# Performance work log

Hardware: AMD Instinct MI355X
Metric: run time of the kernel (lower is better)

Reference implementation:

```python
import jax, jax.numpy as jnp
import numpy as np

B, DIN, DOUT, GRID_SIZE, SPLINE_ORDER, N_LAYERS = 4096, 1024, 1024, 8, 3, 2
COEFFS = GRID_SIZE + SPLINE_ORDER  # 11


def _kaiming_uniform(key, shape, fan_in):
    # torch nn.init.kaiming_uniform_ default: a=0 -> gain=sqrt(2), bound=sqrt(3)*gain/sqrt(fan_in)
    bound = float(np.sqrt(6.0 / fan_in))
    return jax.random.uniform(key, shape, jnp.float32, -bound, bound)


def setup_inputs() -> dict:
    key = jax.random.key(0)
    ks = jax.random.split(key, 1 + 3 * N_LAYERS)
    x = jax.random.normal(ks[0], (B, DIN), dtype=jnp.float32)
    # knot grid: arange(-so, gs+so+1)*h + lo, h=(hi-lo)/gs  -> shape [GRID_SIZE+2*SPLINE_ORDER+1]
    h = 2.0 / GRID_SIZE
    grid = jnp.arange(-SPLINE_ORDER, GRID_SIZE + SPLINE_ORDER + 1, dtype=jnp.float32) * h - 1.0
    base_w, spline_w, scaler = [], [], []
    for i in range(N_LAYERS):
        base_w.append(_kaiming_uniform(ks[1 + 3 * i], (DOUT, DIN), DIN))
        spline_w.append(_kaiming_uniform(ks[2 + 3 * i], (DOUT, DIN, COEFFS), DIN * COEFFS))
        scaler.append(_kaiming_uniform(ks[3 + 3 * i], (DOUT, DIN), DIN))
    return {
        "x": x,
        "base_w": jnp.stack(base_w),      # [L, DOUT, DIN]
        "spline_w": jnp.stack(spline_w),  # [L, DOUT, DIN, COEFFS]
        "scaler": jnp.stack(scaler),      # [L, DOUT, DIN]
        "grid": grid,                      # [G]
        "spline_order": SPLINE_ORDER,
    }


def b_splines(x, grid, spline_order):
    # x: (B, DIN) -> bases: (B, DIN, COEFFS) via Cox-de Boor recursion
    x = x[..., None]  # (B, DIN, 1)
    bases = ((x >= grid[:-1]) & (x < grid[1:])).astype(x.dtype)  # order-0 indicators
    for k in range(1, spline_order + 1):
        left = (x - grid[: -(k + 1)]) / (grid[k:-1] - grid[: -(k + 1)])
        right = (grid[k + 1:] - x) / (grid[k + 1:] - grid[1:-k])
        bases = left * bases[..., :-1] + right * bases[..., 1:]
    return bases


def reference(x, base_w, spline_w, scaler, grid, spline_order):
    so = int(spline_order)
    n_layers = base_w.shape[0]
    for i in range(n_layers):
        x = jax.nn.silu(x)                                  # base_activation applied before both branches
        base_out = x @ base_w[i].T                          # (B, DOUT)
        bs = b_splines(x, grid, so)                         # (B, DIN, COEFFS)
        w = spline_w[i] * scaler[i][..., None]              # (DOUT, DIN, COEFFS)
        spline_out = jnp.einsum("bic,oic->bo", bs, w)      # == F.linear on flattened (DIN*COEFFS)
        x = base_out + spline_out
    return x
```

## Files before the change

kernel.cpp:

```cpp
#include <hip/hip_runtime.h>
#include <stdint.h>

#define BATCH 4096
#define DIN 1024
#define DOUT 1024
#define NC 11
#define KD 12288
#define NKNOTS 15

typedef __bf16 bf16x8 __attribute__((ext_vector_type(8)));
typedef float f32x4 __attribute__((ext_vector_type(4)));

__device__ __forceinline__ unsigned short f2bf(float f) {
    unsigned int u = __float_as_uint(f);
    unsigned int r = (u + 0x7FFFu + ((u >> 16) & 1u)) >> 16;
    return (unsigned short)r;
}

__global__ __launch_bounds__(256) void build_A(
    const float* __restrict__ x, const float* __restrict__ P, int np,
    const float* __restrict__ grid, unsigned short* __restrict__ A) {
    __shared__ __align__(16) unsigned short lbs[256 * NC];
    const int tid = threadIdx.x;
    const int b  = blockIdx.x >> 2;
    const int i0 = (blockIdx.x & 3) * 256;
    const int i  = i0 + tid;

    float g[NKNOTS];
#pragma unroll
    for (int j = 0; j < NKNOTS; ++j) g[j] = grid[j];

    float xv = x[(size_t)b * DIN + i];
    for (int p = 0; p < np; ++p)
        xv += P[(size_t)p * BATCH * DIN + (size_t)b * DIN + i];
    const float s = xv / (1.f + __expf(-xv));

    float bs[14];
#pragma unroll
    for (int c = 0; c < 14; ++c) bs[c] = (s >= g[c] && s < g[c + 1]) ? 1.f : 0.f;
#pragma unroll
    for (int k = 1; k <= 3; ++k) {
        const float inv = (k == 1) ? 4.f : (k == 2) ? 2.f : (4.f / 3.f);
#pragma unroll
        for (int c = 0; c < 14 - k; ++c) {
            float left  = (s - g[c]) * inv;
            float right = (g[c + k + 1] - s) * inv;
            bs[c] = left * bs[c] + right * bs[c + 1];
        }
    }

    A[(size_t)b * KD + i] = f2bf(s);
#pragma unroll
    for (int c = 0; c < NC; ++c) lbs[tid * NC + c] = f2bf(bs[c]);
    __syncthreads();

    const uint4* src = (const uint4*)lbs;
    uint4* dst = (uint4*)(A + (size_t)b * KD + DIN + (size_t)i0 * NC);
    for (int j = tid; j < 352; j += 256) dst[j] = src[j];
}

__global__ __launch_bounds__(256) void build_W(
    const float* __restrict__ base_w, const float* __restrict__ spline_w,
    const float* __restrict__ scaler, unsigned short* __restrict__ W) {
    __shared__ __align__(16) unsigned short lw[256 * NC];
    const int tid = threadIdx.x;
    const int o  = blockIdx.x >> 2;
    const int i0 = (blockIdx.x & 3) * 256;
    const int i  = i0 + tid;
    const size_t oi = (size_t)o * DIN + i;

    const float sc = scaler[oi];
    W[(size_t)o * KD + i] = f2bf(base_w[oi]);
    const float* sw = spline_w + oi * NC;
#pragma unroll
    for (int c = 0; c < NC; ++c) lw[tid * NC + c] = f2bf(sw[c] * sc);
    __syncthreads();

    const uint4* src = (const uint4*)lw;
    uint4* dst = (uint4*)(W + (size_t)o * KD + DIN + (size_t)i0 * NC);
    for (int j = tid; j < 352; j += 256) dst[j] = src[j];
}

#define BM 256
#define BN 256
#define BK 64

#define LOADAF(AF, BASE)                                                       \
    _Pragma("unroll")                                                          \
    for (int fm = 0; fm < 4; ++fm)                                             \
        _Pragma("unroll")                                                      \
        for (int ks = 0; ks < 2; ++ks)                                         \
            AF[fm][ks] = *(const bf16x8*)&(BASE)[(wm * 64 + fm * 16 + rof) * 64 + \
                                                 (((ks * 4 + kcol) ^ xr) * 8)];

#define LOADBF(BF, BASE)                                                       \
    _Pragma("unroll")                                                          \
    for (int fn = 0; fn < 2; ++fn)                                             \
        _Pragma("unroll")                                                      \
        for (int ks = 0; ks < 2; ++ks)                                         \
            BF[fn][ks] = *(const bf16x8*)&(BASE)[(wn * 32 + fn * 16 + rof) * 64 + \
                                                 (((ks * 4 + kcol) ^ xr) * 8)];

#define MFMA16(AF, BF, RO, CO)                                                 \
    __builtin_amdgcn_s_setprio(1);                                             \
    _Pragma("unroll")                                                          \
    for (int ks = 0; ks < 2; ++ks)                                             \
        _Pragma("unroll")                                                      \
        for (int fm = 0; fm < 4; ++fm)                                         \
            _Pragma("unroll")                                                  \
            for (int fn = 0; fn < 2; ++fn)                                     \
                acc[(RO) + fm][(CO) + fn] =                                    \
                    __builtin_amdgcn_mfma_f32_16x16x32_bf16(                   \
                        AF[fm][ks], BF[fn][ks], acc[(RO) + fm][(CO) + fn], 0, 0, 0); \
    __builtin_amdgcn_s_setprio(0);

#define SBAR  __builtin_amdgcn_s_barrier()
#define SCHED __builtin_amdgcn_sched_barrier(0)

__global__ __launch_bounds__(512, 2) void gemm_kan(
    const unsigned short* __restrict__ A,
    const unsigned short* __restrict__ W,
    float* __restrict__ C, float* __restrict__ Part,
    int kspl, int ktper) {
    __shared__ unsigned short As[2 * 2 * 8192];
    __shared__ unsigned short Bs[2 * 2 * 8192];

    const int tid  = threadIdx.x;
    const int wave = tid >> 6;
    const int lane = tid & 63;
    const int per = 16 * kspl;
    const int n0  = (blockIdx.x / per) * BN;
    const int r   = blockIdx.x % per;
    const int ksp = r % kspl;
    const int m0  = (r / kspl) * BM;
    const int wm = wave >> 2;
    const int wn = wave & 3;

    const int srow = lane >> 3;
    const int scol = 8 * ((lane & 7) ^ (lane >> 3));
    const int kbase = ksp * ktper * BK;

    f32x4 acc[8][4];
#pragma unroll
    for (int a = 0; a < 8; ++a)
#pragma unroll
        for (int b = 0; b < 4; ++b) acc[a][b] = (f32x4){0.f, 0.f, 0.f, 0.f};

    auto stageA = [&](int buf, int h, int kt) {
        const int kk = kbase + kt * BK + scol;
#pragma unroll
        for (int c = 0; c < 2; ++c) {
            const int chunk = wave * 2 + c;
            const unsigned short* ga =
                A + (size_t)(m0 + h * 128 + chunk * 8 + srow) * KD + kk;
            __builtin_amdgcn_global_load_lds(
                (const __attribute__((address_space(1))) unsigned int*)ga,
                (__attribute__((address_space(3))) unsigned int*)
                    &As[buf * 16384 + h * 8192 + chunk * 512], 16, 0, 0);
        }
    };
    auto stageB = [&](int buf, int h, int kt) {
        const int kk = kbase + kt * BK + scol;
#pragma unroll
        for (int c = 0; c < 2; ++c) {
            const int chunk = wave * 2 + c;
            const unsigned short* gb =
                W + (size_t)(n0 + h * 128 + chunk * 8 + srow) * KD + kk;
            __builtin_amdgcn_global_load_lds(
                (const __attribute__((address_space(1))) unsigned int*)gb,
                (__attribute__((address_space(3))) unsigned int*)
                    &Bs[buf * 16384 + h * 8192 + chunk * 512], 16, 0, 0);
        }
    };

    stageA(0, 0, 0); stageB(0, 0, 0); stageB(0, 1, 0); stageA(0, 1, 0);
    asm volatile("s_waitcnt vmcnt(0)" ::: "memory");
    SBAR;
    SCHED;

    const int rof  = lane & 15;
    const int xr   = lane & 7;
    const int kcol = lane >> 4;

    bf16x8 af[4][2], b0[2][2], b1[2][2];

    for (int t = 0; t < ktper; ++t) {
        const int cur = t & 1;
        const int nxt = cur ^ 1;
        const bool pf = (t + 1 < ktper);
        const unsigned short* Ab = &As[cur * 16384];
        const unsigned short* Bb = &Bs[cur * 16384];

        LOADAF(af, Ab);
        LOADBF(b0, Bb);
        LOADBF(b1, Bb + 8192);
        if (pf) { stageA(nxt, 0, t + 1); stageB(nxt, 0, t + 1); }
        MFMA16(af, b0, 0, 0);
        if (pf) stageB(nxt, 1, t + 1);
        MFMA16(af, b1, 0, 2);
        LOADAF(af, Ab + 8192);
        if (pf) stageA(nxt, 1, t + 1);
        MFMA16(af, b1, 4, 2);
        MFMA16(af, b0, 4, 0);
        SCHED;
        if (pf) {
            asm volatile("s_waitcnt vmcnt(0)" ::: "memory");
            SBAR;
            SCHED;
        }
    }

    float* Cp = (ksp == 0) ? C : (Part + (size_t)(ksp - 1) * BATCH * DOUT);
    const int crow = (lane >> 4) * 4;
    const int ccol = lane & 15;
#pragma unroll
    for (int H = 0; H < 2; ++H)
#pragma unroll
        for (int fm = 0; fm < 4; ++fm)
#pragma unroll
            for (int F = 0; F < 2; ++F)
#pragma unroll
                for (int fn = 0; fn < 2; ++fn) {
                    const int row = m0 + H * 128 + wm * 64 + fm * 16 + crow;
                    const int col = n0 + F * 128 + wn * 32 + fn * 16 + ccol;
#pragma unroll
                    for (int rr = 0; rr < 4; ++rr)
                        Cp[(size_t)(row + rr) * DOUT + col] =
                            acc[H * 4 + fm][F * 2 + fn][rr];
                }
}

__global__ __launch_bounds__(256) void reduce_add(
    const float* __restrict__ P, float* __restrict__ X, int np) {
    const size_t i = ((size_t)blockIdx.x * 256 + threadIdx.x) * 4;
    f32x4 a = *(const f32x4*)(X + i);
    for (int p = 0; p < np; ++p)
        a = a + *(const f32x4*)(P + (size_t)p * BATCH * DOUT + i);
    *(f32x4*)(X + i) = a;
}

extern "C" void kernel_launch(void* const* d_in, const int* in_sizes, int n_in,
                              void* d_out, int out_size, void* d_ws, size_t ws_size,
                              hipStream_t stream) {
    const float* x        = (const float*)d_in[0];
    const float* base_w   = (const float*)d_in[1];
    const float* spline_w = (const float*)d_in[2];
    const float* scaler   = (const float*)d_in[3];
    const float* grid     = (const float*)d_in[4];
    float* out = (float*)d_out;

    char* ws = (char*)d_ws;
    unsigned short* Abf = (unsigned short*)ws;
    unsigned short* Wbf = (unsigned short*)(ws + 100663296);
    float* xtmp = (float*)(ws + 100663296 + 25165824);
    float* Part = (float*)(ws + 100663296 + 25165824 + 16777216);

    const size_t base_need = 100663296u + 25165824u + 16777216u;
    const int kspl = (ws_size >= base_need + 3u * 16777216u) ? 4 : 2;
    const int ktper = (KD / BK) / kspl;

    for (int layer = 0; layer < 2; ++layer) {
        const float* xin = (layer == 0) ? x : xtmp;
        float* xout      = (layer == 0) ? xtmp : out;
        build_W<<<4096, 256, 0, stream>>>(base_w + (size_t)layer * DOUT * DIN,
                                          spline_w + (size_t)layer * DOUT * DIN * NC,
                                          scaler + (size_t)layer * DOUT * DIN, Wbf);
        build_A<<<16384, 256, 0, stream>>>(xin, Part, (layer == 0) ? 0 : kspl - 1,
                                           grid, Abf);
        gemm_kan<<<64 * kspl, 512, 0, stream>>>(Abf, Wbf, xout, Part, kspl, ktper);
    }
    reduce_add<<<BATCH * DOUT / 1024, 256, 0, stream>>>(Part, out, kspl - 1);
}
```

Before: 275.0 us.

## Switch GEMM to 256x128x32 tiles with 4-wave blocks and new LDS swizzle

```diff
diff --git a/kernel.cpp b/kernel.cpp
--- a/kernel.cpp
+++ b/kernel.cpp
@@ -82,48 +82,30 @@
 }
 
 #define BM 256
-#define BN 256
-#define BK 64
-
-#define LOADAF(AF, BASE)                                                       \
+#define BN 128
+#define BK 32
+
+#define MFMA8(AF, BF, RO, FN0)                                                 \
+    __builtin_amdgcn_s_setprio(1);                                             \
     _Pragma("unroll")                                                          \
     for (int fm = 0; fm < 4; ++fm)                                             \
         _Pragma("unroll")                                                      \
-        for (int ks = 0; ks < 2; ++ks)                                         \
-            AF[fm][ks] = *(const bf16x8*)&(BASE)[(wm * 64 + fm * 16 + rof) * 64 + \
-                                                 (((ks * 4 + kcol) ^ xr) * 8)];
-
-#define LOADBF(BF, BASE)                                                       \
-    _Pragma("unroll")                                                          \
-    for (int fn = 0; fn < 2; ++fn)                                             \
-        _Pragma("unroll")                                                      \
-        for (int ks = 0; ks < 2; ++ks)                                         \
-            BF[fn][ks] = *(const bf16x8*)&(BASE)[(wn * 32 + fn * 16 + rof) * 64 + \
-                                                 (((ks * 4 + kcol) ^ xr) * 8)];
-
-#define MFMA16(AF, BF, RO, CO)                                                 \
-    __builtin_amdgcn_s_setprio(1);                                             \
-    _Pragma("unroll")                                                          \
-    for (int ks = 0; ks < 2; ++ks)                                             \
-        _Pragma("unroll")                                                      \
-        for (int fm = 0; fm < 4; ++fm)                                         \
-            _Pragma("unroll")                                                  \
-            for (int fn = 0; fn < 2; ++fn)                                     \
-                acc[(RO) + fm][(CO) + fn] =                                    \
-                    __builtin_amdgcn_mfma_f32_16x16x32_bf16(                   \
-                        AF[fm][ks], BF[fn][ks], acc[(RO) + fm][(CO) + fn], 0, 0, 0); \
+        for (int fn = 0; fn < 2; ++fn)                                         \
+            acc[(RO) + fm][(FN0) + fn] =                                       \
+                __builtin_amdgcn_mfma_f32_16x16x32_bf16(                       \
+                    AF[fm], BF[(FN0) + fn], acc[(RO) + fm][(FN0) + fn], 0, 0, 0); \
     __builtin_amdgcn_s_setprio(0);
 
 #define SBAR  __builtin_amdgcn_s_barrier()
 #define SCHED __builtin_amdgcn_sched_barrier(0)
 
-__global__ __launch_bounds__(512, 2) void gemm_kan(
+__global__ __launch_bounds__(256, 2) void gemm_kan(
     const unsigned short* __restrict__ A,
     const unsigned short* __restrict__ W,
     float* __restrict__ C, float* __restrict__ Part,
     int kspl, int ktper) {
-    __shared__ unsigned short As[2 * 2 * 8192];
-    __shared__ unsigned short Bs[2 * 2 * 8192];
+    __shared__ unsigned short As[2 * 8192];
+    __shared__ unsigned short Bs[2 * 4096];
 
     const int tid  = threadIdx.x;
     const int wave = tid >> 6;
@@ -133,11 +115,13 @@
     const int r   = blockIdx.x % per;
     const int ksp = r % kspl;
     const int m0  = (r / kspl) * BM;
-    const int wm = wave >> 2;
-    const int wn = wave & 3;
-
-    const int srow = lane >> 3;
-    const int scol = 8 * ((lane & 7) ^ (lane >> 3));
+    const int wm = wave >> 1;
+    const int wn = wave & 1;
+
+    const int srow2 = lane >> 3;
+    const int sl8g  = (lane & 7) ^ srow2;
+    const int sgrow = 2 * srow2 + (sl8g >> 2);
+    const int sgcol = (sl8g & 3) * 8;
     const int kbase = ksp * ktper * BK;
 
     f32x4 acc[8][4];
@@ -146,62 +130,65 @@
 #pragma unroll
         for (int b = 0; b < 4; ++b) acc[a][b] = (f32x4){0.f, 0.f, 0.f, 0.f};
 
-    auto stageA = [&](int buf, int h, int kt) {
-        const int kk = kbase + kt * BK + scol;
-#pragma unroll
-        for (int c = 0; c < 2; ++c) {
-            const int chunk = wave * 2 + c;
-            const unsigned short* ga =
-                A + (size_t)(m0 + h * 128 + chunk * 8 + srow) * KD + kk;
-            __builtin_amdgcn_global_load_lds(
-                (const __attribute__((address_space(1))) unsigned int*)ga,
-                (__attribute__((address_space(3))) unsigned int*)
-                    &As[buf * 16384 + h * 8192 + chunk * 512], 16, 0, 0);
-        }
+    auto stageA = [&](int buf, int kt, int c) {
+        const int chunk = wave * 4 + c;
+        const unsigned short* ga =
+            A + (size_t)(m0 + chunk * 16 + sgrow) * KD + kbase + kt * BK + sgcol;
+        __builtin_amdgcn_global_load_lds(
+            (const __attribute__((address_space(1))) unsigned int*)ga,
+            (__attribute__((address_space(3))) unsigned int*)
+                &As[buf * 8192 + chunk * 512], 16, 0, 0);
     };
-    auto stageB = [&](int buf, int h, int kt) {
-        const int kk = kbase + kt * BK + scol;
-#pragma unroll
-        for (int c = 0; c < 2; ++c) {
-            const int chunk = wave * 2 + c;
-            const unsigned short* gb =
-                W + (size_t)(n0 + h * 128 + chunk * 8 + srow) * KD + kk;
-            __builtin_amdgcn_global_load_lds(
-                (const __attribute__((address_space(1))) unsigned int*)gb,
-                (__attribute__((address_space(3))) unsigned int*)
-                    &Bs[buf * 16384 + h * 8192 + chunk * 512], 16, 0, 0);
-        }
+    auto stageB = [&](int buf, int kt, int c) {
+        const int chunk = wave * 2 + c;
+        const unsigned short* gb =
+            W + (size_t)(n0 + chunk * 16 + sgrow) * KD + kbase + kt * BK + sgcol;
+        __builtin_amdgcn_global_load_lds(
+            (const __attribute__((address_space(1))) unsigned int*)gb,
+            (__attribute__((address_space(3))) unsigned int*)
+                &Bs[buf * 4096 + chunk * 512], 16, 0, 0);
     };
 
-    stageA(0, 0, 0); stageB(0, 0, 0); stageB(0, 1, 0); stageA(0, 1, 0);
+    const int rof  = lane & 15;
+    const int kcol = lane >> 4;
+    const int sl8r = (4 * (rof & 1) + kcol) ^ (rof >> 1);
+    const int lanebase = (rof >> 1) * 64 + sl8r * 8;
+
+#define LOADAF(AF, H)                                                          \
+    _Pragma("unroll")                                                          \
+    for (int fm = 0; fm < 4; ++fm)                                             \
+        AF[fm] = *(const bf16x8*)&As[cur * 8192 +                              \
+                     (wm * 128 + (H) * 64 + fm * 16) * 32 + lanebase];
+
+#define LOADB(BF)                                                              \
+    _Pragma("unroll")                                                          \
+    for (int fn = 0; fn < 4; ++fn)                                             \
+        BF[fn] = *(const bf16x8*)&Bs[cur * 4096 +                              \
+                     (wn * 64 + fn * 16) * 32 + lanebase];
+
+    for (int c = 0; c < 4; ++c) stageA(0, 0, c);
+    for (int c = 0; c < 2; ++c) stageB(0, 0, c);
     asm volatile("s_waitcnt vmcnt(0)" ::: "memory");
     SBAR;
     SCHED;
 
-    const int rof  = lane & 15;
-    const int xr   = lane & 7;
-    const int kcol = lane >> 4;
-
-    bf16x8 af[4][2], b0[2][2], b1[2][2];
+    bf16x8 af[4], bf[4];
 
     for (int t = 0; t < ktper; ++t) {
         const int cur = t & 1;
         const int nxt = cur ^ 1;
         const bool pf = (t + 1 < ktper);
-        const unsigned short* Ab = &As[cur * 16384];
-        const unsigned short* Bb = &Bs[cur * 16384];
-
-        LOADAF(af, Ab);
-        LOADBF(b0, Bb);
-        LOADBF(b1, Bb + 8192);
-        if (pf) { stageA(nxt, 0, t + 1); stageB(nxt, 0, t + 1); }
-        MFMA16(af, b0, 0, 0);
-        if (pf) stageB(nxt, 1, t + 1);
-        MFMA16(af, b1, 0, 2);
-        LOADAF(af, Ab + 8192);
-        if (pf) stageA(nxt, 1, t + 1);
-        MFMA16(af, b1, 4, 2);
-        MFMA16(af, b0, 4, 0);
+
+        LOADAF(af, 0);
+        LOADB(bf);
+        if (pf) { stageA(nxt, t + 1, 0); stageA(nxt, t + 1, 1); }
+        MFMA8(af, bf, 0, 0);
+        if (pf) { stageA(nxt, t + 1, 2); stageA(nxt, t + 1, 3); }
+        MFMA8(af, bf, 0, 2);
+        LOADAF(af, 1);
+        if (pf) { stageB(nxt, t + 1, 0); stageB(nxt, t + 1, 1); }
+        MFMA8(af, bf, 4, 0);
+        MFMA8(af, bf, 4, 2);
         SCHED;
         if (pf) {
             asm volatile("s_waitcnt vmcnt(0)" ::: "memory");
@@ -218,16 +205,14 @@
 #pragma unroll
         for (int fm = 0; fm < 4; ++fm)
 #pragma unroll
-            for (int F = 0; F < 2; ++F)
-#pragma unroll
-                for (int fn = 0; fn < 2; ++fn) {
-                    const int row = m0 + H * 128 + wm * 64 + fm * 16 + crow;
-                    const int col = n0 + F * 128 + wn * 32 + fn * 16 + ccol;
-#pragma unroll
-                    for (int rr = 0; rr < 4; ++rr)
-                        Cp[(size_t)(row + rr) * DOUT + col] =
-                            acc[H * 4 + fm][F * 2 + fn][rr];
-                }
+            for (int fn = 0; fn < 4; ++fn) {
+                const int row = m0 + wm * 128 + H * 64 + fm * 16 + crow;
+                const int col = n0 + wn * 64 + fn * 16 + ccol;
+#pragma unroll
+                for (int rr = 0; rr < 4; ++rr)
+                    Cp[(size_t)(row + rr) * DOUT + col] =
+                        acc[H * 4 + fm][fn][rr];
+            }
 }
 
 __global__ __launch_bounds__(256) void reduce_add(
@@ -267,7 +252,7 @@
                                           scaler + (size_t)layer * DOUT * DIN, Wbf);
         build_A<<<16384, 256, 0, stream>>>(xin, Part, (layer == 0) ? 0 : kspl - 1,
                                            grid, Abf);
-        gemm_kan<<<64 * kspl, 512, 0, stream>>>(Abf, Wbf, xout, Part, kspl, ktper);
+        gemm_kan<<<128 * kspl, 256, 0, stream>>>(Abf, Wbf, xout, Part, kspl, ktper);
     }
     reduce_add<<<BATCH * DOUT / 1024, 256, 0, stream>>>(Part, out, kspl - 1);
 }
```

Measured after the change: 318.7 us. 1.16x slower.
